# Kernel tuning notes

Hardware: AMD Instinct MI355X
Metric: run time of the kernel (lower is better)

The kernel has to match this reference:

```python
import jax, jax.numpy as jnp
import numpy as np

D_MODEL = 512
HEAD = 64

def setup_inputs() -> dict:
    key = jax.random.key(0)
    ks = jax.random.split(key, 7)
    s_in = 1.0 / np.sqrt(D_MODEL)
    x = jax.random.normal(ks[0], (4, 4096, D_MODEL), dtype=jnp.float32)
    Wk = jax.random.uniform(ks[1], (D_MODEL, HEAD), jnp.float32, -s_in, s_in)
    bk = jax.random.uniform(ks[2], (HEAD,), jnp.float32, -s_in, s_in)
    Wq = jax.random.uniform(ks[3], (D_MODEL, HEAD), jnp.float32, -s_in, s_in)
    bq = jax.random.uniform(ks[4], (HEAD,), jnp.float32, -s_in, s_in)
    Wv = jax.random.uniform(ks[5], (D_MODEL, HEAD), jnp.float32, -s_in, s_in)
    bv = jax.random.uniform(ks[6], (HEAD,), jnp.float32, -s_in, s_in)
    return {"x": x, "Wk": Wk, "bk": bk, "Wq": Wq, "bq": bq, "Wv": Wv, "bv": bv}

def reference(x, Wk, bk, Wq, bq, Wv, bv):
    B, T, C = x.shape
    k = x @ Wk + bk            # [B,T,H]
    q = x @ Wq + bq            # [B,T,H]
    v = x @ Wv + bv            # [B,T,H]
    scale = C ** (-0.5)
    # NOTE: original computes k @ q^T (keys index rows), softmax over query axis
    w = jnp.einsum('bkh,bqh->bkq', k, q) * scale  # [B,T,T]
    w = jax.nn.softmax(w, axis=-1)
    out = jnp.einsum('bkq,bqh->bkh', w, v)        # [B,T,H]
    return out
```

## Files before the change

### kernel.cpp

```cpp
#include <hip/hip_runtime.h>


#define DM 512
#define HD 64
#define TSEQ 4096
#define KSCALE (1.4426950408889634f * 0.04419417382415922f)

typedef __attribute__((ext_vector_type(8))) __bf16 bf16x8;
typedef __attribute__((ext_vector_type(4))) __bf16 bf16x4;
typedef __attribute__((ext_vector_type(4))) float f32x4;
typedef __attribute__((ext_vector_type(16))) float f32x16;
typedef __attribute__((ext_vector_type(4))) unsigned int uint4v;

__device__ __forceinline__ float fast_exp2(float x) {
#if __has_builtin(__builtin_amdgcn_exp2f)
    return __builtin_amdgcn_exp2f(x);
#else
    return exp2f(x);
#endif
}

__device__ __forceinline__ bf16x8 ld_bf16x8(const unsigned short* p) {
    return __builtin_bit_cast(bf16x8, *(const uint4v*)p);
}
__device__ __forceinline__ f32x4 mfma16(bf16x8 a, bf16x8 b, f32x4 c) {
    return __builtin_amdgcn_mfma_f32_16x16x32_bf16(a, b, c, 0, 0, 0);
}
__device__ __forceinline__ f32x16 mfma32(bf16x8 a, bf16x8 b, f32x16 c) {
    return __builtin_amdgcn_mfma_f32_32x32x16_bf16(a, b, c, 0, 0, 0);
}

typedef const __attribute__((address_space(1))) unsigned int* gas_t;
typedef __attribute__((address_space(3))) unsigned int* las_t;
__device__ __forceinline__ void async_cp16(const void* g, void* l) {
    __builtin_amdgcn_global_load_lds((gas_t)(unsigned long long)g,
                                     (las_t)(unsigned int)(unsigned long long)l,
                                     16, 0, 0);
}

__global__ __launch_bounds__(256) void prep_wt(const float* __restrict__ Wk,
                                               const float* __restrict__ Wq,
                                               const float* __restrict__ Wv,
                                               unsigned short* __restrict__ WT) {
    int e = blockIdx.x * 256 + threadIdx.x;
    int m = e >> 15;
    int idx = e & 32767;
    int h = idx >> 9;
    int cc = idx & 511;
    const float* W = (m == 0) ? Wk : ((m == 1) ? Wq : Wv);
    float v = W[cc * HD + h];
    if (m == 0) v *= KSCALE;
    ((__bf16*)WT)[m * 32768 + h * DM + cc] = (__bf16)v;
}

__global__ __launch_bounds__(512, 4) void proj(const float* __restrict__ x,
                                               const unsigned short* __restrict__ WT,
                                               const float* __restrict__ bk,
                                               const float* __restrict__ bq,
                                               const float* __restrict__ bv,
                                               unsigned short* __restrict__ Kw,
                                               unsigned short* __restrict__ Qw,
                                               unsigned short* __restrict__ VTw) {
    __shared__ alignas(16) float xs[32 * 64];
    const int tid = threadIdx.x;
    const int wv = tid >> 6, lane = tid & 63;
    const int c = lane & 15, quad = lane >> 4;
    const int ng = wv & 3, rg = wv >> 2;
    const int bx = blockIdx.x;
    const int n0 = ng * 16;

    const int row_s = tid >> 4, p_s = tid & 15;
    const char* xg = (const char*)x + (size_t)(bx * 32 + row_s) * 2048
                   + ((p_s ^ (row_s & 15)) * 16);
    char* xls = (char*)xs + wv * 1024;

    const int arow = rg * 16 + c;
    int aoff[2][2];
#pragma unroll
    for (int ks = 0; ks < 2; ++ks)
#pragma unroll
        for (int b = 0; b < 2; ++b)
            aoff[ks][b] = arow * 256 + (((ks * 8 + quad * 2 + b) ^ (arow & 15)) * 16);

    const unsigned short* wtb = WT + (n0 + c) * DM + quad * 8;

    f32x4 acc[3];
#pragma unroll
    for (int m = 0; m < 3; ++m) acc[m] = (f32x4){0.f, 0.f, 0.f, 0.f};

    for (int kt = 0; kt < 8; ++kt) {
        __syncthreads();
        async_cp16(xg + kt * 256, xls);
        __builtin_amdgcn_s_waitcnt(0x0f70);
        __syncthreads();
#pragma unroll
        for (int ks = 0; ks < 2; ++ks) {
            f32x4 xa = *(const f32x4*)((const char*)xs + aoff[ks][0]);
            f32x4 xb = *(const f32x4*)((const char*)xs + aoff[ks][1]);
            bf16x8 af;
            af[0] = (__bf16)xa[0]; af[1] = (__bf16)xa[1]; af[2] = (__bf16)xa[2]; af[3] = (__bf16)xa[3];
            af[4] = (__bf16)xb[0]; af[5] = (__bf16)xb[1]; af[6] = (__bf16)xb[2]; af[7] = (__bf16)xb[3];
#pragma unroll
            for (int m = 0; m < 3; ++m) {
                bf16x8 bf = ld_bf16x8(wtb + m * 32768 + kt * 64 + ks * 32);
                acc[m] = mfma16(af, bf, acc[m]);
            }
        }
    }

    const int row0 = bx * 32 + rg * 16 + quad * 4;
#pragma unroll
    for (int m = 0; m < 3; ++m) {
        const float* bp = (m == 0) ? bk : ((m == 1) ? bq : bv);
        float bias = bp[n0 + c];
        if (m == 0) bias *= KSCALE;
        if (m < 2) {
            __bf16* dst = (__bf16*)((m == 0) ? Kw : Qw);
#pragma unroll
            for (int r = 0; r < 4; ++r)
                dst[(row0 + r) * HD + n0 + c] = (__bf16)(acc[m][r] + bias);
        } else {
            bf16x4 pk;
#pragma unroll
            for (int r = 0; r < 4; ++r) pk[r] = (__bf16)(acc[m][r] + bias);
            int b = bx >> 7;
            int rowb = (bx & 127) * 32 + rg * 16 + quad * 4;
            *(bf16x4*)(VTw + ((size_t)(b * 64 + n0 + c)) * TSEQ + rowb) = pk;
        }
    }
}

__global__ __launch_bounds__(512, 4) void attn(const unsigned short* __restrict__ Kw,
                                               const unsigned short* __restrict__ Qw,
                                               const unsigned short* __restrict__ VTw,
                                               float* __restrict__ Op,
                                               float* __restrict__ Lp) {
    __shared__ alignas(16) char smem[51200];
    __shared__ float lds_l[8][32];
    unsigned short* QL = (unsigned short*)smem;
    unsigned short* VL = (unsigned short*)(smem + 16384);
    unsigned short* PL = (unsigned short*)(smem + 32768);
    float* OC = (float*)smem;

    const int tid = threadIdx.x;
    const int wv = tid >> 6, lane = tid & 63;
    const int l5 = lane >> 5, l31 = lane & 31;
    const int rg = wv >> 2, jc = wv & 3;
    const int bx = blockIdx.x;
    const int js = bx & 1, tile = (bx >> 1) & 63, batch = bx >> 7;

    const int irow = batch * TSEQ + tile * 64 + rg * 32 + l31;
    bf16x8 kf[4];
#pragma unroll
    for (int ks = 0; ks < 4; ++ks) kf[ks] = ld_bf16x8(Kw + irow * HD + ks * 16 + l5 * 8);

    const int qrow = jc * 32 + l31;
    int qoff[4];
#pragma unroll
    for (int ks = 0; ks < 4; ++ks)
        qoff[ks] = qrow * 128 + (((ks * 2 + l5) ^ (qrow & 7)) * 16);
    int voff[2][2];
#pragma unroll
    for (int ht = 0; ht < 2; ++ht)
#pragma unroll
        for (int ks = 0; ks < 2; ++ks) {
            int h = ht * 32 + l31;
            voff[ht][ks] = h * 256 + (((jc * 4 + ks * 2 + l5) ^ (h & 15)) * 16);
        }
    unsigned short* Pw = PL + wv * 1152;

    const char* qg = (const char*)(Qw + (size_t)(batch * TSEQ + js * 2048) * HD);
    const char* vg = (const char*)(VTw + (size_t)batch * 64 * TSEQ + js * 2048);
    const int L1 = 512 + tid;
    const int qgo0 = ((tid >> 3) * 128) + (((tid & 7) ^ ((tid >> 3) & 7)) * 16);
    const int qgo1 = ((L1 >> 3) * 128) + (((L1 & 7) ^ ((L1 >> 3) & 7)) * 16);
    const int vgo0 = ((tid >> 4) * 8192) + (((tid & 15) ^ ((tid >> 4) & 15)) * 16);
    const int vgo1 = ((L1 >> 4) * 8192) + (((L1 & 15) ^ ((L1 >> 4) & 15)) * 16);
    char* qls0 = smem + wv * 1024;
    char* qls1 = smem + 8192 + wv * 1024;
    char* vls0 = smem + 16384 + wv * 1024;
    char* vls1 = smem + 16384 + 8192 + wv * 1024;

    f32x16 o0, o1;
#pragma unroll
    for (int r = 0; r < 16; ++r) { o0[r] = 0.f; o1[r] = 0.f; }
    float l_acc = 0.f;

    for (int jt = 0; jt < 16; ++jt) {
        __syncthreads();
        async_cp16(qg + jt * 16384 + qgo0, qls0);
        async_cp16(qg + jt * 16384 + qgo1, qls1);
        async_cp16(vg + jt * 256 + vgo0, vls0);
        async_cp16(vg + jt * 256 + vgo1, vls1);
        __builtin_amdgcn_s_waitcnt(0x0f70);
        __syncthreads();

        f32x16 s;
#pragma unroll
        for (int r = 0; r < 16; ++r) s[r] = 0.f;
#pragma unroll
        for (int ks = 0; ks < 4; ++ks) {
            bf16x8 qa = ld_bf16x8((const unsigned short*)((const char*)QL + qoff[ks]));
            s = mfma32(qa, kf[ks], s);
        }

        float p[16];
#pragma unroll
        for (int r = 0; r < 16; ++r) p[r] = fast_exp2(s[r]);
        l_acc += ((p[0] + p[1]) + (p[2] + p[3])) + ((p[4] + p[5]) + (p[6] + p[7]))
               + ((p[8] + p[9]) + (p[10] + p[11])) + ((p[12] + p[13]) + (p[14] + p[15]));
#pragma unroll
        for (int rq = 0; rq < 4; ++rq) {
            bf16x4 w;
            w[0] = (__bf16)p[rq * 4 + 0]; w[1] = (__bf16)p[rq * 4 + 1];
            w[2] = (__bf16)p[rq * 4 + 2]; w[3] = (__bf16)p[rq * 4 + 3];
            *(bf16x4*)(Pw + l31 * 36 + rq * 8 + l5 * 4) = w;
        }

        bf16x8 pb[2];
#pragma unroll
        for (int ks = 0; ks < 2; ++ks) {
            bf16x4 lo = *(const bf16x4*)(Pw + l31 * 36 + ks * 16 + l5 * 8);
            bf16x4 hi = *(const bf16x4*)(Pw + l31 * 36 + ks * 16 + l5 * 8 + 4);
            bf16x8 t;
            t[0] = lo[0]; t[1] = lo[1]; t[2] = lo[2]; t[3] = lo[3];
            t[4] = hi[0]; t[5] = hi[1]; t[6] = hi[2]; t[7] = hi[3];
            pb[ks] = t;
        }

#pragma unroll
        for (int ks = 0; ks < 2; ++ks) {
            bf16x8 vf0 = ld_bf16x8((const unsigned short*)((const char*)VL + voff[0][ks]));
            bf16x8 vf1 = ld_bf16x8((const unsigned short*)((const char*)VL + voff[1][ks]));
            o0 = mfma32(vf0, pb[ks], o0);
            o1 = mfma32(vf1, pb[ks], o1);
        }
    }

    l_acc += __shfl_xor(l_acc, 32, 64);
    if (lane < 32) lds_l[wv][l31] = l_acc;

#pragma unroll
    for (int ht = 0; ht < 2; ++ht) {
        __syncthreads();
        f32x16 o = ht ? o1 : o0;
#pragma unroll
        for (int r = 0; r < 16; ++r) {
            int hh = (r & 3) + 8 * (r >> 2) + 4 * l5;
            OC[((rg * 4 + jc) * 32 + hh) * 32 + l31] = o[r];
        }
        __syncthreads();
        {
            int rg2 = tid >> 8;
            int i2 = (tid >> 3) & 31;
            int h4 = (tid & 7) * 4;
            f32x4 a4 = {0.f, 0.f, 0.f, 0.f};
#pragma unroll
            for (int j2 = 0; j2 < 4; ++j2)
#pragma unroll
                for (int k = 0; k < 4; ++k)
                    a4[k] += OC[((rg2 * 4 + j2) * 32 + h4 + k) * 32 + i2];
            int row = batch * TSEQ + tile * 64 + rg2 * 32 + i2;
            *(f32x4*)(Op + (size_t)js * 1048576 + (size_t)row * HD + ht * 32 + h4) = a4;
        }
        if (ht == 0 && tid < 64) {
            int rg2 = tid >> 5, i2 = tid & 31;
            float L = lds_l[rg2 * 4 + 0][i2] + lds_l[rg2 * 4 + 1][i2]
                    + lds_l[rg2 * 4 + 2][i2] + lds_l[rg2 * 4 + 3][i2];
            int row = batch * TSEQ + tile * 64 + rg2 * 32 + i2;
            Lp[js * 16384 + row] = L;
        }
    }
}

__global__ __launch_bounds__(512) void fin(const float* __restrict__ Op,
                                           const float* __restrict__ Lp,
                                           float* __restrict__ out) {
    int idx = blockIdx.x * 512 + threadIdx.x;
    int e = idx * 4;
    int row = e >> 6;
    f32x4 a = *(const f32x4*)(Op + e);
    f32x4 b = *(const f32x4*)(Op + 1048576 + e);
    float L = Lp[row] + Lp[16384 + row];
    f32x4 r;
#pragma unroll
    for (int k = 0; k < 4; ++k) r[k] = (a[k] + b[k]) / L;
    *(f32x4*)(out + e) = r;
}

extern "C" void kernel_launch(void* const* d_in, const int* in_sizes, int n_in,
                              void* d_out, int out_size, void* d_ws, size_t ws_size,
                              hipStream_t stream) {
    (void)in_sizes; (void)n_in; (void)out_size; (void)ws_size;
    const float* x  = (const float*)d_in[0];
    const float* Wk = (const float*)d_in[1];
    const float* bk = (const float*)d_in[2];
    const float* Wq = (const float*)d_in[3];
    const float* bq = (const float*)d_in[4];
    const float* Wv = (const float*)d_in[5];
    const float* bv = (const float*)d_in[6];

    char* ws = (char*)d_ws;
    unsigned short* WT  = (unsigned short*)(ws);
    unsigned short* Kw  = (unsigned short*)(ws + 196608);
    unsigned short* Qw  = (unsigned short*)(ws + 2293760);
    unsigned short* VTw = (unsigned short*)(ws + 4390912);
    float* Opart        = (float*)(ws + 6488064);
    float* Lpart        = (float*)(ws + 14876672);
    float* outp = (float*)d_out;

    hipLaunchKernelGGL(prep_wt, dim3(384), dim3(256), 0, stream, Wk, Wq, Wv, WT);
    hipLaunchKernelGGL(proj, dim3(512), dim3(512), 0, stream,
                       x, WT, bk, bq, bv, Kw, Qw, VTw);
    hipLaunchKernelGGL(attn, dim3(512), dim3(512), 0, stream, Kw, Qw, VTw, Opart, Lpart);
    hipLaunchKernelGGL(fin, dim3(512), dim3(512), 0, stream, Opart, Lpart, outp);
}
```

Measured before the change: 139.5 us.

## Double-buffer attention tiles, widen row tile, shuffle P in registers, preload x

The attention kernel now handles 128 key rows per block instead of 64, so each loaded Q/V tile is reused for twice as many rows, and the grid drops to 256 blocks. Q/V tiles are double-buffered with async copies issued one iteration ahead, and the P matrix goes from the C layout to the B-operand layout through cross-lane shuffles instead of an LDS round trip. The projection kernel loads its whole 32x512 x tile into LDS once rather than in eight synchronised chunks. In exchange there is more register pressure (four output accumulators), lower occupancy (launch bound 2), and fewer blocks than CUs on a 256-CU part.

```diff
diff --git a/kernel.cpp b/kernel.cpp
--- a/kernel.cpp
+++ b/kernel.cpp
@@ -8,6 +8,7 @@
 
 typedef __attribute__((ext_vector_type(8))) __bf16 bf16x8;
 typedef __attribute__((ext_vector_type(4))) __bf16 bf16x4;
+typedef __attribute__((ext_vector_type(2))) __bf16 bf16x2;
 typedef __attribute__((ext_vector_type(4))) float f32x4;
 typedef __attribute__((ext_vector_type(16))) float f32x16;
 typedef __attribute__((ext_vector_type(4))) unsigned int uint4v;
@@ -61,7 +62,7 @@
                                                unsigned short* __restrict__ Kw,
                                                unsigned short* __restrict__ Qw,
                                                unsigned short* __restrict__ VTw) {
-    __shared__ alignas(16) float xs[32 * 64];
+    __shared__ alignas(16) float xs[16384];
     const int tid = threadIdx.x;
     const int wv = tid >> 6, lane = tid & 63;
     const int c = lane & 15, quad = lane >> 4;
@@ -69,42 +70,37 @@
     const int bx = blockIdx.x;
     const int n0 = ng * 16;
 
-    const int row_s = tid >> 4, p_s = tid & 15;
-    const char* xg = (const char*)x + (size_t)(bx * 32 + row_s) * 2048
-                   + ((p_s ^ (row_s & 15)) * 16);
-    char* xls = (char*)xs + wv * 1024;
+#pragma unroll
+    for (int r = 0; r < 8; ++r) {
+        int cid = r * 512 + tid;
+        int row = cid >> 7, pos = cid & 127;
+        int g = (pos & ~7) | ((pos ^ row) & 7);
+        async_cp16((const char*)x + (size_t)(bx * 32 + row) * 2048 + g * 16,
+                   (char*)xs + r * 8192 + wv * 1024);
+    }
+    __builtin_amdgcn_s_waitcnt(0x0f70);
+    __syncthreads();
 
     const int arow = rg * 16 + c;
-    int aoff[2][2];
-#pragma unroll
-    for (int ks = 0; ks < 2; ++ks)
-#pragma unroll
-        for (int b = 0; b < 2; ++b)
-            aoff[ks][b] = arow * 256 + (((ks * 8 + quad * 2 + b) ^ (arow & 15)) * 16);
-
     const unsigned short* wtb = WT + (n0 + c) * DM + quad * 8;
-
     f32x4 acc[3];
 #pragma unroll
     for (int m = 0; m < 3; ++m) acc[m] = (f32x4){0.f, 0.f, 0.f, 0.f};
 
-    for (int kt = 0; kt < 8; ++kt) {
-        __syncthreads();
-        async_cp16(xg + kt * 256, xls);
-        __builtin_amdgcn_s_waitcnt(0x0f70);
-        __syncthreads();
-#pragma unroll
-        for (int ks = 0; ks < 2; ++ks) {
-            f32x4 xa = *(const f32x4*)((const char*)xs + aoff[ks][0]);
-            f32x4 xb = *(const f32x4*)((const char*)xs + aoff[ks][1]);
-            bf16x8 af;
-            af[0] = (__bf16)xa[0]; af[1] = (__bf16)xa[1]; af[2] = (__bf16)xa[2]; af[3] = (__bf16)xa[3];
-            af[4] = (__bf16)xb[0]; af[5] = (__bf16)xb[1]; af[6] = (__bf16)xb[2]; af[7] = (__bf16)xb[3];
-#pragma unroll
-            for (int m = 0; m < 3; ++m) {
-                bf16x8 bf = ld_bf16x8(wtb + m * 32768 + kt * 64 + ks * 32);
-                acc[m] = mfma16(af, bf, acc[m]);
-            }
+#pragma unroll
+    for (int ks = 0; ks < 16; ++ks) {
+        int p0 = ks * 8 + quad * 2;
+        int sp0 = (p0 & ~7) | ((p0 ^ arow) & 7);
+        int sp1 = ((p0 + 1) & ~7) | (((p0 + 1) ^ arow) & 7);
+        f32x4 xa = *(const f32x4*)((const char*)xs + arow * 2048 + sp0 * 16);
+        f32x4 xb = *(const f32x4*)((const char*)xs + arow * 2048 + sp1 * 16);
+        bf16x8 af;
+        af[0] = (__bf16)xa[0]; af[1] = (__bf16)xa[1]; af[2] = (__bf16)xa[2]; af[3] = (__bf16)xa[3];
+        af[4] = (__bf16)xb[0]; af[5] = (__bf16)xb[1]; af[6] = (__bf16)xb[2]; af[7] = (__bf16)xb[3];
+#pragma unroll
+        for (int m = 0; m < 3; ++m) {
+            bf16x8 bf = ld_bf16x8(wtb + m * 32768 + ks * 32);
+            acc[m] = mfma16(af, bf, acc[m]);
         }
     }
 
@@ -130,44 +126,42 @@
     }
 }
 
-__global__ __launch_bounds__(512, 4) void attn(const unsigned short* __restrict__ Kw,
+__global__ __launch_bounds__(512, 2) void attn(const unsigned short* __restrict__ Kw,
                                                const unsigned short* __restrict__ Qw,
                                                const unsigned short* __restrict__ VTw,
                                                float* __restrict__ Op,
                                                float* __restrict__ Lp) {
-    __shared__ alignas(16) char smem[51200];
-    __shared__ float lds_l[8][32];
-    unsigned short* QL = (unsigned short*)smem;
-    unsigned short* VL = (unsigned short*)(smem + 16384);
-    unsigned short* PL = (unsigned short*)(smem + 32768);
-    float* OC = (float*)smem;
+    __shared__ alignas(16) char smem[65536];
 
     const int tid = threadIdx.x;
     const int wv = tid >> 6, lane = tid & 63;
     const int l5 = lane >> 5, l31 = lane & 31;
     const int rg = wv >> 2, jc = wv & 3;
     const int bx = blockIdx.x;
-    const int js = bx & 1, tile = (bx >> 1) & 63, batch = bx >> 7;
-
-    const int irow = batch * TSEQ + tile * 64 + rg * 32 + l31;
-    bf16x8 kf[4];
-#pragma unroll
-    for (int ks = 0; ks < 4; ++ks) kf[ks] = ld_bf16x8(Kw + irow * HD + ks * 16 + l5 * 8);
-
-    const int qrow = jc * 32 + l31;
+    const int batch = bx >> 6, js = (bx >> 5) & 1, tile = bx & 31;
+    const int rowbase = batch * TSEQ + tile * 128;
+
+    bf16x8 kf[2][4];
+#pragma unroll
+    for (int it = 0; it < 2; ++it) {
+        const unsigned short* kp = Kw + (size_t)(rowbase + rg * 64 + it * 32 + l31) * HD;
+#pragma unroll
+        for (int ks = 0; ks < 4; ++ks) kf[it][ks] = ld_bf16x8(kp + ks * 16 + l5 * 8);
+    }
+
+    const int jrow = jc * 32 + l31;
     int qoff[4];
 #pragma unroll
     for (int ks = 0; ks < 4; ++ks)
-        qoff[ks] = qrow * 128 + (((ks * 2 + l5) ^ (qrow & 7)) * 16);
+        qoff[ks] = jrow * 128 + (((ks * 2 + l5) ^ (jrow & 7)) * 16);
     int voff[2][2];
 #pragma unroll
     for (int ht = 0; ht < 2; ++ht)
 #pragma unroll
-        for (int ks = 0; ks < 2; ++ks) {
+        for (int k2 = 0; k2 < 2; ++k2) {
             int h = ht * 32 + l31;
-            voff[ht][ks] = h * 256 + (((jc * 4 + ks * 2 + l5) ^ (h & 15)) * 16);
-        }
-    unsigned short* Pw = PL + wv * 1152;
+            voff[ht][k2] = h * 256 + (((jc * 4 + k2 * 2 + l5) ^ (h & 15)) * 16);
+        }
 
     const char* qg = (const char*)(Qw + (size_t)(batch * TSEQ + js * 2048) * HD);
     const char* vg = (const char*)(VTw + (size_t)batch * 64 * TSEQ + js * 2048);
@@ -176,99 +170,128 @@
     const int qgo1 = ((L1 >> 3) * 128) + (((L1 & 7) ^ ((L1 >> 3) & 7)) * 16);
     const int vgo0 = ((tid >> 4) * 8192) + (((tid & 15) ^ ((tid >> 4) & 15)) * 16);
     const int vgo1 = ((L1 >> 4) * 8192) + (((L1 & 15) ^ ((L1 >> 4) & 15)) * 16);
-    char* qls0 = smem + wv * 1024;
-    char* qls1 = smem + 8192 + wv * 1024;
-    char* vls0 = smem + 16384 + wv * 1024;
-    char* vls1 = smem + 16384 + 8192 + wv * 1024;
-
-    f32x16 o0, o1;
-#pragma unroll
-    for (int r = 0; r < 16; ++r) { o0[r] = 0.f; o1[r] = 0.f; }
-    float l_acc = 0.f;
+
+    f32x16 o00, o01, o10, o11;
+#pragma unroll
+    for (int r = 0; r < 16; ++r) { o00[r] = 0.f; o01[r] = 0.f; o10[r] = 0.f; o11[r] = 0.f; }
+    float lac0 = 0.f, lac1 = 0.f;
+
+    {
+        char* nb = smem;
+        async_cp16(qg + qgo0, nb + wv * 1024);
+        async_cp16(qg + qgo1, nb + 8192 + wv * 1024);
+        async_cp16(vg + vgo0, nb + 16384 + wv * 1024);
+        async_cp16(vg + vgo1, nb + 16384 + 8192 + wv * 1024);
+    }
 
     for (int jt = 0; jt < 16; ++jt) {
-        __syncthreads();
-        async_cp16(qg + jt * 16384 + qgo0, qls0);
-        async_cp16(qg + jt * 16384 + qgo1, qls1);
-        async_cp16(vg + jt * 256 + vgo0, vls0);
-        async_cp16(vg + jt * 256 + vgo1, vls1);
         __builtin_amdgcn_s_waitcnt(0x0f70);
         __syncthreads();
-
-        f32x16 s;
-#pragma unroll
-        for (int r = 0; r < 16; ++r) s[r] = 0.f;
+        const char* cb = smem + (jt & 1) * 32768;
+        if (jt < 15) {
+            char* nb = smem + ((jt + 1) & 1) * 32768;
+            async_cp16(qg + (jt + 1) * 16384 + qgo0, nb + wv * 1024);
+            async_cp16(qg + (jt + 1) * 16384 + qgo1, nb + 8192 + wv * 1024);
+            async_cp16(vg + (jt + 1) * 256 + vgo0, nb + 16384 + wv * 1024);
+            async_cp16(vg + (jt + 1) * 256 + vgo1, nb + 16384 + 8192 + wv * 1024);
+            __builtin_amdgcn_sched_barrier(0);
+        }
+        const unsigned short* QL = (const unsigned short*)cb;
+        const unsigned short* VL = (const unsigned short*)(cb + 16384);
+
+        f32x16 s0, s1;
+#pragma unroll
+        for (int r = 0; r < 16; ++r) { s0[r] = 0.f; s1[r] = 0.f; }
 #pragma unroll
         for (int ks = 0; ks < 4; ++ks) {
             bf16x8 qa = ld_bf16x8((const unsigned short*)((const char*)QL + qoff[ks]));
-            s = mfma32(qa, kf[ks], s);
-        }
-
-        float p[16];
-#pragma unroll
-        for (int r = 0; r < 16; ++r) p[r] = fast_exp2(s[r]);
-        l_acc += ((p[0] + p[1]) + (p[2] + p[3])) + ((p[4] + p[5]) + (p[6] + p[7]))
-               + ((p[8] + p[9]) + (p[10] + p[11])) + ((p[12] + p[13]) + (p[14] + p[15]));
-#pragma unroll
-        for (int rq = 0; rq < 4; ++rq) {
-            bf16x4 w;
-            w[0] = (__bf16)p[rq * 4 + 0]; w[1] = (__bf16)p[rq * 4 + 1];
-            w[2] = (__bf16)p[rq * 4 + 2]; w[3] = (__bf16)p[rq * 4 + 3];
-            *(bf16x4*)(Pw + l31 * 36 + rq * 8 + l5 * 4) = w;
-        }
-
-        bf16x8 pb[2];
-#pragma unroll
-        for (int ks = 0; ks < 2; ++ks) {
-            bf16x4 lo = *(const bf16x4*)(Pw + l31 * 36 + ks * 16 + l5 * 8);
-            bf16x4 hi = *(const bf16x4*)(Pw + l31 * 36 + ks * 16 + l5 * 8 + 4);
-            bf16x8 t;
-            t[0] = lo[0]; t[1] = lo[1]; t[2] = lo[2]; t[3] = lo[3];
-            t[4] = hi[0]; t[5] = hi[1]; t[6] = hi[2]; t[7] = hi[3];
-            pb[ks] = t;
-        }
-
-#pragma unroll
-        for (int ks = 0; ks < 2; ++ks) {
-            bf16x8 vf0 = ld_bf16x8((const unsigned short*)((const char*)VL + voff[0][ks]));
-            bf16x8 vf1 = ld_bf16x8((const unsigned short*)((const char*)VL + voff[1][ks]));
-            o0 = mfma32(vf0, pb[ks], o0);
-            o1 = mfma32(vf1, pb[ks], o1);
-        }
-    }
-
-    l_acc += __shfl_xor(l_acc, 32, 64);
-    if (lane < 32) lds_l[wv][l31] = l_acc;
-
-#pragma unroll
-    for (int ht = 0; ht < 2; ++ht) {
+            s0 = mfma32(qa, kf[0][ks], s0);
+            s1 = mfma32(qa, kf[1][ks], s1);
+        }
+
+        unsigned int pk0[8], pk1[8];
+#pragma unroll
+        for (int m = 0; m < 8; ++m) {
+            float a0 = fast_exp2(s0[2 * m]), a1 = fast_exp2(s0[2 * m + 1]);
+            float b0 = fast_exp2(s1[2 * m]), b1 = fast_exp2(s1[2 * m + 1]);
+            lac0 += a0 + a1;
+            lac1 += b0 + b1;
+            bf16x2 ta; ta[0] = (__bf16)a0; ta[1] = (__bf16)a1;
+            bf16x2 tb; tb[0] = (__bf16)b0; tb[1] = (__bf16)b1;
+            pk0[m] = __builtin_bit_cast(unsigned int, ta);
+            pk1[m] = __builtin_bit_cast(unsigned int, tb);
+        }
+
+#pragma unroll
+        for (int k2 = 0; k2 < 2; ++k2) {
+            bf16x8 pb0, pb1;
+            {
+                unsigned int A0 = pk0[k2 * 4 + 0], A1 = pk0[k2 * 4 + 1];
+                unsigned int B0 = pk0[k2 * 4 + 2], B1 = pk0[k2 * 4 + 3];
+                unsigned int t0 = l5 ? A0 : B0, t1 = l5 ? A1 : B1;
+                unsigned int r0 = (unsigned int)__shfl_xor((int)t0, 32, 64);
+                unsigned int r1 = (unsigned int)__shfl_xor((int)t1, 32, 64);
+                uint4v u;
+                u[0] = l5 ? r0 : A0; u[1] = l5 ? r1 : A1;
+                u[2] = l5 ? B0 : r0; u[3] = l5 ? B1 : r1;
+                pb0 = __builtin_bit_cast(bf16x8, u);
+            }
+            {
+                unsigned int A0 = pk1[k2 * 4 + 0], A1 = pk1[k2 * 4 + 1];
+                unsigned int B0 = pk1[k2 * 4 + 2], B1 = pk1[k2 * 4 + 3];
+                unsigned int t0 = l5 ? A0 : B0, t1 = l5 ? A1 : B1;
+                unsigned int r0 = (unsigned int)__shfl_xor((int)t0, 32, 64);
+                unsigned int r1 = (unsigned int)__shfl_xor((int)t1, 32, 64);
+                uint4v u;
+                u[0] = l5 ? r0 : A0; u[1] = l5 ? r1 : A1;
+                u[2] = l5 ? B0 : r0; u[3] = l5 ? B1 : r1;
+                pb1 = __builtin_bit_cast(bf16x8, u);
+            }
+            bf16x8 vf0 = ld_bf16x8((const unsigned short*)((const char*)VL + voff[0][k2]));
+            bf16x8 vf1 = ld_bf16x8((const unsigned short*)((const char*)VL + voff[1][k2]));
+            o00 = mfma32(vf0, pb0, o00);
+            o01 = mfma32(vf0, pb1, o01);
+            o10 = mfma32(vf1, pb0, o10);
+            o11 = mfma32(vf1, pb1, o11);
+        }
+    }
+
+    lac0 += __shfl_xor(lac0, 32, 64);
+    lac1 += __shfl_xor(lac1, 32, 64);
+    __syncthreads();
+    float* OCp = (float*)smem;
+    float* ldsl = (float*)(smem + 34816);
+    if (l5 == 0) {
+        ldsl[jc * 128 + rg * 64 + l31] = lac0;
+        ldsl[jc * 128 + rg * 64 + 32 + l31] = lac1;
+    }
+
+#pragma unroll
+    for (int ph = 0; ph < 4; ++ph) {
+        const int ht = ph >> 1, ih = ph & 1;
         __syncthreads();
-        f32x16 o = ht ? o1 : o0;
-#pragma unroll
-        for (int r = 0; r < 16; ++r) {
-            int hh = (r & 3) + 8 * (r >> 2) + 4 * l5;
-            OC[((rg * 4 + jc) * 32 + hh) * 32 + l31] = o[r];
+        if (rg == ih) {
+            const f32x16 oa = ht ? o10 : o00;
+            const f32x16 ob = ht ? o11 : o01;
+#pragma unroll
+            for (int r = 0; r < 16; ++r) {
+                int hr = (r & 3) + 8 * (r >> 2) + 4 * l5;
+                OCp[(jc * 32 + hr) * 68 + l31] = oa[r];
+                OCp[(jc * 32 + hr) * 68 + 32 + l31] = ob[r];
+            }
         }
         __syncthreads();
-        {
-            int rg2 = tid >> 8;
-            int i2 = (tid >> 3) & 31;
-            int h4 = (tid & 7) * 4;
-            f32x4 a4 = {0.f, 0.f, 0.f, 0.f};
-#pragma unroll
-            for (int j2 = 0; j2 < 4; ++j2)
-#pragma unroll
-                for (int k = 0; k < 4; ++k)
-                    a4[k] += OC[((rg2 * 4 + j2) * 32 + h4 + k) * 32 + i2];
-            int row = batch * TSEQ + tile * 64 + rg2 * 32 + i2;
-            *(f32x4*)(Op + (size_t)js * 1048576 + (size_t)row * HD + ht * 32 + h4) = a4;
-        }
-        if (ht == 0 && tid < 64) {
-            int rg2 = tid >> 5, i2 = tid & 31;
-            float L = lds_l[rg2 * 4 + 0][i2] + lds_l[rg2 * 4 + 1][i2]
-                    + lds_l[rg2 * 4 + 2][i2] + lds_l[rg2 * 4 + 3][i2];
-            int row = batch * TSEQ + tile * 64 + rg2 * 32 + i2;
-            Lp[js * 16384 + row] = L;
+#pragma unroll
+        for (int rep = 0; rep < 4; ++rep) {
+            int idx = rep * 512 + tid;
+            int i = idx >> 5, hr = idx & 31;
+            float v = OCp[(0 * 32 + hr) * 68 + i] + OCp[(1 * 32 + hr) * 68 + i]
+                    + OCp[(2 * 32 + hr) * 68 + i] + OCp[(3 * 32 + hr) * 68 + i];
+            Op[(size_t)js * 1048576 + (size_t)(rowbase + ih * 64 + i) * HD + ht * 32 + hr] = v;
+        }
+        if (ph == 0 && tid < 128) {
+            float L = ldsl[tid] + ldsl[128 + tid] + ldsl[256 + tid] + ldsl[384 + tid];
+            Lp[js * 16384 + rowbase + tid] = L;
         }
     }
 }
@@ -312,6 +335,6 @@
     hipLaunchKernelGGL(prep_wt, dim3(384), dim3(256), 0, stream, Wk, Wq, Wv, WT);
     hipLaunchKernelGGL(proj, dim3(512), dim3(512), 0, stream,
                        x, WT, bk, bq, bv, Kw, Qw, VTw);
-    hipLaunchKernelGGL(attn, dim3(512), dim3(512), 0, stream, Kw, Qw, VTw, Opart, Lpart);
+    hipLaunchKernelGGL(attn, dim3(256), dim3(512), 0, stream, Kw, Qw, VTw, Opart, Lpart);
     hipLaunchKernelGGL(fin, dim3(512), dim3(512), 0, stream, Opart, Lpart, outp);
 }
```

Result: no change. 137.3 us (-1.6%).
